# Kernel tuning notes

Measured on AMD Instinct MI355X. Metric: run time of the kernel, lower is better.

## Reference

```python
import jax, jax.numpy as jnp
import numpy as np

ALPHA = 0.2  # leakyrelu negative slope
NEG_INF = -1.0e12


def setup_inputs() -> dict:
    key = jax.random.key(0)
    k1, k2, k3, k4, k5 = jax.random.split(key, 5)
    B, N, C_in, C_out = 8, 2048, 256, 256
    inp = jax.random.normal(k1, (B, N, C_in), dtype=jnp.float32)
    adj = jax.random.randint(k2, (N, N), 0, 2, dtype=jnp.int32)
    # xavier_uniform with gain=1.414 for (C_in, C_out)
    limit = 1.414 * np.sqrt(6.0 / (C_in + C_out))
    W1 = jax.random.uniform(k3, (C_in, C_out), jnp.float32, -limit, limit)
    W2 = jax.random.uniform(k4, (C_in, C_out), jnp.float32, -limit, limit)
    W3 = jax.random.uniform(k5, (C_in, C_out), jnp.float32, -limit, limit)
    return {"inp": inp, "adj": adj, "W1": W1, "W2": W2, "W3": W3}


def reference(inp, adj, W1, W2, W3):
    # inp: [B,N,Cin], adj: [N,N], W*: [Cin,Cout]
    h1 = jnp.einsum('bnc,cd->bnd', inp, W1)  # [B,N,Cout] queries
    h2 = jnp.einsum('bnc,cd->bnd', inp, W2)  # [B,N,Cout] keys
    h3 = jnp.einsum('bnc,cd->bnd', inp, W3)  # [B,N,Cout] values
    e = jnp.einsum('bnd,bmd->bnm', h1, h2)   # [B,N,N] scores
    e = jax.nn.leaky_relu(e, ALPHA)
    e = jnp.where(adj[None, :, :] > 0, e, NEG_INF)
    attention = jax.nn.softmax(e, axis=-1)   # dropout p=0 / eval mode -> identity
    h_prime = jnp.einsum('bnm,bmd->bnd', attention, h3)
    return jax.nn.relu(h_prime)  # concat=True
```

## Files before the change

### kernel.cpp

```cpp
#include <hip/hip_runtime.h>

typedef __bf16 bf16_t;
typedef __bf16 bf16x4 __attribute__((ext_vector_type(4)));
typedef __bf16 bf16x8 __attribute__((ext_vector_type(8)));
typedef float floatx4 __attribute__((ext_vector_type(4)));
typedef signed char i8_t;
typedef int intx4 __attribute__((ext_vector_type(4)));

__device__ inline void split_hl(float v, bf16_t& hi, bf16_t& lo) {
    hi = (bf16_t)v;
    lo = (bf16_t)(v - (float)hi);
}

__global__ void adjbits_kernel(const int* __restrict__ adj, unsigned* __restrict__ bits) {
    int id = blockIdx.x * 256 + threadIdx.x;
    const int* p = adj + (size_t)id * 32;
    unsigned w = 0;
#pragma unroll
    for (int j = 0; j < 32; j += 4) {
        int4 v = *(const int4*)(p + j);
        w |= (v.x > 0 ? 1u : 0u) << j;
        w |= (v.y > 0 ? 1u : 0u) << (j + 1);
        w |= (v.z > 0 ? 1u : 0u) << (j + 2);
        w |= (v.w > 0 ? 1u : 0u) << (j + 3);
    }
    bits[id] = w;
}

__global__ void wtrans_kernel(const float* __restrict__ W1,
                              const float* __restrict__ W2,
                              const float* __restrict__ W3,
                              bf16_t* __restrict__ Wthi, bf16_t* __restrict__ Wtlo) {
    __shared__ float T[64 * 68];
    const int zi = blockIdx.z;
    const float* W = (zi == 0) ? W1 : ((zi == 1) ? W2 : W3);
    bf16_t* ohi = Wthi + zi * 256 * 256;
    bf16_t* olo = Wtlo + zi * 256 * 256;
    const int c0 = blockIdx.x * 64, d0 = blockIdx.y * 64;
    const int tid = threadIdx.x;
#pragma unroll
    for (int i = 0; i < 4; i++) {
        int idx = i * 256 + tid;
        int r = idx >> 4, c4 = (idx & 15) * 4;
        floatx4 v = *(const floatx4*)(W + (c0 + r) * 256 + d0 + c4);
        *(floatx4*)(&T[r * 68 + c4]) = v;
    }
    __syncthreads();
#pragma unroll
    for (int i = 0; i < 4; i++) {
        int idx = i * 256 + tid;
        int rd = idx & 63, cc4 = (idx >> 6) * 4;
        bf16x4 vh, vl;
#pragma unroll
        for (int ii = 0; ii < 4; ii++) {
            float v = T[(cc4 + ii) * 68 + rd];
            bf16_t h, l; split_hl(v, h, l);
            vh[ii] = h; vl[ii] = l;
        }
        *(bf16x4*)(ohi + (d0 + rd) * 256 + c0 + cc4) = vh;
        *(bf16x4*)(olo + (d0 + rd) * 256 + c0 + cc4) = vl;
    }
}

__global__ __launch_bounds__(256) void proj_kernel(
    const float* __restrict__ X,
    const bf16_t* __restrict__ Wthi, const bf16_t* __restrict__ Wtlo,
    i8_t* __restrict__ Q8h, i8_t* __restrict__ Q8l, float* __restrict__ sqv,
    i8_t* __restrict__ K8h, i8_t* __restrict__ K8l, float* __restrict__ skv,
    bf16_t* __restrict__ H3t) {
    __shared__ bf16_t Xh[64 * 40], Xl[64 * 40];
    __shared__ bf16_t Wh[256 * 40], Wl[256 * 40];
    const int z = blockIdx.y;
    const int row0 = blockIdx.x * 64;
    const int tid = threadIdx.x;
    const int w = tid >> 6, lane = tid & 63;
    const int m = lane & 15, q = lane >> 4;
    const bf16_t* Wzh = Wthi + z * 256 * 256;
    const bf16_t* Wzl = Wtlo + z * 256 * 256;

    floatx4 acc[16];
#pragma unroll
    for (int i = 0; i < 16; i++) acc[i] = (floatx4){0.f, 0.f, 0.f, 0.f};

    for (int c0 = 0; c0 < 256; c0 += 32) {
#pragma unroll
        for (int i = 0; i < 2; i++) {
            int idx = i * 256 + tid;
            int r = idx >> 3, c4 = (idx & 7) * 4;
            floatx4 v = *(const floatx4*)(X + (size_t)(row0 + r) * 256 + c0 + c4);
            bf16x4 vh, vl;
#pragma unroll
            for (int ii = 0; ii < 4; ii++) {
                bf16_t h, l; split_hl(v[ii], h, l);
                vh[ii] = h; vl[ii] = l;
            }
            *(bf16x4*)(&Xh[r * 40 + c4]) = vh;
            *(bf16x4*)(&Xl[r * 40 + c4]) = vl;
        }
#pragma unroll
        for (int i = 0; i < 4; i++) {
            int idx = i * 256 + tid;
            int d = idx >> 2, c8 = (idx & 3) * 8;
            *(bf16x8*)(&Wh[d * 40 + c8]) = *(const bf16x8*)(Wzh + d * 256 + c0 + c8);
            *(bf16x8*)(&Wl[d * 40 + c8]) = *(const bf16x8*)(Wzl + d * 256 + c0 + c8);
        }
        __syncthreads();
        bf16x8 ah = *(const bf16x8*)(&Xh[(w * 16 + m) * 40 + q * 8]);
        bf16x8 al = *(const bf16x8*)(&Xl[(w * 16 + m) * 40 + q * 8]);
#pragma unroll
        for (int nt = 0; nt < 16; nt++) {
            bf16x8 bh = *(const bf16x8*)(&Wh[(nt * 16 + m) * 40 + q * 8]);
            bf16x8 bl = *(const bf16x8*)(&Wl[(nt * 16 + m) * 40 + q * 8]);
            acc[nt] = __builtin_amdgcn_mfma_f32_16x16x32_bf16(ah, bh, acc[nt], 0, 0, 0);
            acc[nt] = __builtin_amdgcn_mfma_f32_16x16x32_bf16(ah, bl, acc[nt], 0, 0, 0);
            acc[nt] = __builtin_amdgcn_mfma_f32_16x16x32_bf16(al, bh, acc[nt], 0, 0, 0);
        }
        __syncthreads();
    }
    const int rbase = row0 + w * 16 + q * 4;
    if (z < 2) {
        i8_t* Dh = (z == 0) ? Q8h : K8h;
        i8_t* Dl = (z == 0) ? Q8l : K8l;
        float* sv = (z == 0) ? sqv : skv;
        float am[4] = {0.f, 0.f, 0.f, 0.f};
#pragma unroll
        for (int nt = 0; nt < 16; nt++)
#pragma unroll
            for (int r = 0; r < 4; r++) am[r] = fmaxf(am[r], fabsf(acc[nt][r]));
#pragma unroll
        for (int off = 1; off < 16; off <<= 1)
#pragma unroll
            for (int r = 0; r < 4; r++)
                am[r] = fmaxf(am[r], __shfl_xor(am[r], off, 64));
        float sc[4], inv[4];
#pragma unroll
        for (int r = 0; r < 4; r++) {
            sc[r]  = (am[r] > 0.f) ? am[r] * (1.f / 127.f) : 1.f;
            inv[r] = (am[r] > 0.f) ? 127.f / am[r] : 0.f;
        }
#pragma unroll
        for (int nt = 0; nt < 16; nt++)
#pragma unroll
            for (int r = 0; r < 4; r++) {
                float vq = acc[nt][r] * inv[r];
                float qh = rintf(vq);
                float ql = fminf(fmaxf(rintf((vq - qh) * 256.f), -127.f), 127.f);
                int offo = (rbase + r) * 256 + nt * 16 + m;
                Dh[offo] = (i8_t)(int)qh;
                Dl[offo] = (i8_t)(int)ql;
            }
        if (m == 0) {
#pragma unroll
            for (int r = 0; r < 4; r++) sv[rbase + r] = sc[r];
        }
    } else {
#pragma unroll
        for (int nt = 0; nt < 16; nt++)
#pragma unroll
            for (int r = 0; r < 4; r++) {
                int token = rbase + r;
                int b = token >> 11, n = token & 2047;
                H3t[(size_t)(b * 256 + nt * 16 + m) * 2048 + n] = (bf16_t)acc[nt][r];
            }
    }
}

#define K8SW(row, off) ((off) ^ (((row) & 7) << 4))
#define PSW(row, off)  ((off) ^ ((((row) >> 1) & 3) << 4))
__global__ __launch_bounds__(256, 2) void attn_kernel(
    const i8_t* __restrict__ Q8h, const i8_t* __restrict__ Q8l,
    const float* __restrict__ sqv,
    const i8_t* __restrict__ K8h, const i8_t* __restrict__ K8l,
    const float* __restrict__ skv,
    const bf16_t* __restrict__ H3t, const unsigned* __restrict__ adjbits,
    float* __restrict__ Opart, float* __restrict__ mpart, float* __restrict__ lpart,
    int klen) {
    __shared__ i8_t K8[2][32 * 256];
    __shared__ bf16_t Pl[4][16 * 32];
    __shared__ __align__(16) float Al[4][16];
    __shared__ __align__(16) int Fl[4];

    const int nwg = (int)(gridDim.x * gridDim.y * gridDim.z);
    const int wgid = (int)(blockIdx.x + (blockIdx.y << 5) + (blockIdx.z << 8));
    const int nid = (wgid & 7) * (nwg >> 3) + (wgid >> 3);
    const int qblk = nid & 31;
    const int b  = (nid >> 5) & 7;
    const int kz = nid >> 8;

    const int q0 = qblk * 64;
    const int tid = threadIdx.x;
    const int w = tid >> 6, lane = tid & 63;
    const int m = lane & 15, q = lane >> 4;

    char* K8B0 = (char*)&K8[0][0];
    char* K8B1 = (char*)&K8[1][0];
    char* PlB  = (char*)&Pl[w][0];

    const i8_t* qrh = Q8h + (size_t)(b * 2048 + q0 + w * 16 + m) * 256;
    const i8_t* qrl = Q8l + (size_t)(b * 2048 + q0 + w * 16 + m) * 256;
    intx4 qh8[4], ql8[4];
#pragma unroll
    for (int ck = 0; ck < 4; ck++) {
        qh8[ck] = *(const intx4*)(qrh + ck * 64 + q * 16);
        ql8[ck] = *(const intx4*)(qrl + ck * 64 + q * 16);
    }
    float sq4[4];
#pragma unroll
    for (int r = 0; r < 4; r++) sq4[r] = sqv[b * 2048 + q0 + w * 16 + q * 4 + r];

    bf16x8 vones;
#pragma unroll
    for (int i = 0; i < 8; i++) vones[i] = (bf16_t)1.0f;

    float m_run[4];
#pragma unroll
    for (int r = 0; r < 4; r++) m_run[r] = -3.0e38f;
    floatx4 l_acc = (floatx4){0.f, 0.f, 0.f, 0.f};
    floatx4 o[16];
#pragma unroll
    for (int i = 0; i < 16; i++) o[i] = (floatx4){0.f, 0.f, 0.f, 0.f};

    const unsigned* bitrow[4];
#pragma unroll
    for (int r = 0; r < 4; r++)
        bitrow[r] = adjbits + (size_t)(q0 + w * 16 + q * 4 + r) * 64;

    const bf16_t* vbase = H3t + (size_t)(b * 256 + w * 64 + m) * 2048 + q * 8;

    intx4 rkh[2], rkl[2];
    bf16x8 vcur[4], vnxt[4];
    float skt[2], skn[2];
    const int kbeg = kz * klen, kend = kbeg + klen;

#pragma unroll
    for (int i = 0; i < 2; i++) {
        int ci = i * 256 + tid;
        int kr = ci >> 4, cb = (ci & 15) * 16;
        rkh[i] = *(const intx4*)(K8h + (size_t)(b * 2048 + kbeg + kr) * 256 + cb);
        rkl[i] = *(const intx4*)(K8l + (size_t)(b * 2048 + kbeg + kr) * 256 + cb);
    }
#pragma unroll
    for (int dn = 0; dn < 4; dn++)
        vcur[dn] = *(const bf16x8*)(vbase + (size_t)(dn * 16) * 2048 + kbeg);
    skt[0] = skv[b * 2048 + kbeg + m];
    skt[1] = skv[b * 2048 + kbeg + 16 + m];

    for (int k0 = kbeg; k0 < kend; k0 += 32) {
        __syncthreads();
#pragma unroll
        for (int i = 0; i < 2; i++) {
            int ci = i * 256 + tid;
            int kr = ci >> 4, cb = (ci & 15) * 16;
            *(intx4*)(K8B0 + K8SW(kr, kr * 256 + cb)) = rkh[i];
            *(intx4*)(K8B1 + K8SW(kr, kr * 256 + cb)) = rkl[i];
        }
        __syncthreads();
        if (k0 + 32 < kend) {
            int kn = k0 + 32;
#pragma unroll
            for (int i = 0; i < 2; i++) {
                int ci = i * 256 + tid;
                int kr = ci >> 4, cb = (ci & 15) * 16;
                rkh[i] = *(const intx4*)(K8h + (size_t)(b * 2048 + kn + kr) * 256 + cb);
                rkl[i] = *(const intx4*)(K8l + (size_t)(b * 2048 + kn + kr) * 256 + cb);
            }
#pragma unroll
            for (int dn = 0; dn < 4; dn++)
                vnxt[dn] = *(const bf16x8*)(vbase + (size_t)(dn * 16) * 2048 + kn);
            skn[0] = skv[b * 2048 + kn + m];
            skn[1] = skv[b * 2048 + kn + 16 + m];
        }

        float s[2][4];
#pragma unroll
        for (int t = 0; t < 2; t++) {
            intx4 ch = {0, 0, 0, 0}, cm = {0, 0, 0, 0};
            const int row = t * 16 + m;
#pragma unroll
            for (int ck = 0; ck < 4; ck++) {
                const int cb2 = ck * 64 + q * 16;
                intx4 kh = *(const intx4*)(K8B0 + K8SW(row, row * 256 + cb2));
                intx4 kl = *(const intx4*)(K8B1 + K8SW(row, row * 256 + cb2));
                ch = __builtin_amdgcn_mfma_i32_16x16x64_i8(qh8[ck], kh, ch, 0, 0, 0);
                cm = __builtin_amdgcn_mfma_i32_16x16x64_i8(qh8[ck], kl, cm, 0, 0, 0);
                cm = __builtin_amdgcn_mfma_i32_16x16x64_i8(ql8[ck], kh, cm, 0, 0, 0);
            }
#pragma unroll
            for (int r = 0; r < 4; r++)
                s[t][r] = fmaf((float)cm[r], 0.00390625f, (float)ch[r]) * (sq4[r] * skt[t]);
        }

        unsigned aw[4];
#pragma unroll
        for (int r = 0; r < 4; r++) aw[r] = bitrow[r][k0 >> 5];
        float p[2][4], tmax[4];
#pragma unroll
        for (int r = 0; r < 4; r++) tmax[r] = -3.0e38f;
#pragma unroll
        for (int t = 0; t < 2; t++)
#pragma unroll
            for (int r = 0; r < 4; r++) {
                float v = s[t][r];
                v = (v > 0.f) ? v : 0.2f * v;
                v = ((aw[r] >> (t * 16 + m)) & 1u) ? v : -1.0e12f;
                p[t][r] = v;
                tmax[r] = fmaxf(tmax[r], v);
            }
#pragma unroll
        for (int off = 1; off < 16; off <<= 1)
#pragma unroll
            for (int r = 0; r < 4; r++)
                tmax[r] = fmaxf(tmax[r], __shfl_xor(tmax[r], off, 64));

        int rise = 0;
        float mnew[4];
#pragma unroll
        for (int r = 0; r < 4; r++) {
            mnew[r] = fmaxf(m_run[r], tmax[r]);
            rise |= (mnew[r] > m_run[r]);
        }
        const int rose = __any(rise);
        if (rose) {
            floatx4 a4;
#pragma unroll
            for (int r = 0; r < 4; r++) {
                float alpha = __expf(m_run[r] - mnew[r]);
                m_run[r] = mnew[r];
                l_acc[r] *= alpha;
                a4[r] = alpha;
            }
            if (m == 0) *(floatx4*)(&Al[w][q * 4]) = a4;
        }
        if (lane == 0) Fl[w] = rose;
#pragma unroll
        for (int t = 0; t < 2; t++)
#pragma unroll
            for (int r = 0; r < 4; r++)
                p[t][r] = __expf(p[t][r] - m_run[r]);

#pragma unroll
        for (int t = 0; t < 2; t++)
#pragma unroll
            for (int r = 0; r < 4; r++) {
                int row = q * 4 + r;
                *(bf16_t*)(PlB + PSW(row, row * 64 + (t * 16 + m) * 2)) = (bf16_t)p[t][r];
            }
        __syncthreads();

        int4 fl4 = *(const int4*)(&Fl[0]);
#pragma unroll
        for (int qb = 0; qb < 4; qb++) {
            int f = (qb == 0) ? fl4.x : (qb == 1) ? fl4.y : (qb == 2) ? fl4.z : fl4.w;
            if (f) {
                floatx4 a = *(const floatx4*)(&Al[qb][q * 4]);
#pragma unroll
                for (int dn = 0; dn < 4; dn++)
#pragma unroll
                    for (int r = 0; r < 4; r++) o[qb * 4 + dn][r] *= a[r];
            }
        }

        bf16x8 pa[4];
#pragma unroll
        for (int qb = 0; qb < 4; qb++)
            pa[qb] = *(const bf16x8*)((char*)&Pl[qb][0] + PSW(m, m * 64 + q * 16));
#pragma unroll
        for (int qb = 0; qb < 4; qb++)
            if (qb == w)
                l_acc = __builtin_amdgcn_mfma_f32_16x16x32_bf16(pa[qb], vones, l_acc, 0, 0, 0);
#pragma unroll
        for (int qb = 0; qb < 4; qb++)
#pragma unroll
            for (int dn = 0; dn < 4; dn++)
                o[qb * 4 + dn] = __builtin_amdgcn_mfma_f32_16x16x32_bf16(
                    pa[qb], vcur[dn], o[qb * 4 + dn], 0, 0, 0);

#pragma unroll
        for (int dn = 0; dn < 4; dn++) vcur[dn] = vnxt[dn];
        skt[0] = skn[0];
        skt[1] = skn[1];
    }

    const int rowbase = kz * 16384 + b * 2048 + q0;
#pragma unroll
    for (int qb = 0; qb < 4; qb++)
#pragma unroll
        for (int dn = 0; dn < 4; dn++)
#pragma unroll
            for (int r = 0; r < 4; r++)
                Opart[(size_t)(rowbase + qb * 16 + q * 4 + r) * 256 + w * 64 + dn * 16 + m] =
                    o[qb * 4 + dn][r];
    if (m == 0) {
        const int rowg = rowbase + w * 16 + q * 4;
#pragma unroll
        for (int r = 0; r < 4; r++) {
            mpart[rowg + r] = m_run[r];
            lpart[rowg + r] = l_acc[r];
        }
    }
}

__global__ __launch_bounds__(256) void merge_kernel(
    const float* __restrict__ Opart, const float* __restrict__ mpart,
    const float* __restrict__ lpart, float* __restrict__ out, int S) {
    int gid = blockIdx.x * 256 + threadIdx.x;
    int row = gid >> 6, c4 = (gid & 63) * 4;
    float M = -3.0e38f;
    for (int s = 0; s < S; s++) M = fmaxf(M, mpart[s * 16384 + row]);
    float denom = 0.f;
    float4 acc = make_float4(0.f, 0.f, 0.f, 0.f);
    for (int s = 0; s < S; s++) {
        float sc = __expf(mpart[s * 16384 + row] - M);
        denom += lpart[s * 16384 + row] * sc;
        float4 v = *(const float4*)(Opart + ((size_t)(s * 16384 + row)) * 256 + c4);
        acc.x += v.x * sc; acc.y += v.y * sc; acc.z += v.z * sc; acc.w += v.w * sc;
    }
    float inv = 1.f / denom;
    float4 r;
    r.x = fmaxf(acc.x * inv, 0.f);
    r.y = fmaxf(acc.y * inv, 0.f);
    r.z = fmaxf(acc.z * inv, 0.f);
    r.w = fmaxf(acc.w * inv, 0.f);
    *(float4*)(out + (size_t)row * 256 + c4) = r;
}

extern "C" void kernel_launch(void* const* d_in, const int* in_sizes, int n_in,
                              void* d_out, int out_size, void* d_ws, size_t ws_size,
                              hipStream_t stream) {
    const float* X   = (const float*)d_in[0];
    const int*   adj = (const int*)d_in[1];
    const float* W1  = (const float*)d_in[2];
    const float* W2  = (const float*)d_in[3];
    const float* W3  = (const float*)d_in[4];
    float* out = (float*)d_out;

    char* ws = (char*)d_ws;
    i8_t* Q8h = (i8_t*)(ws + ((size_t)0 << 20));
    i8_t* Q8l = (i8_t*)(ws + ((size_t)4 << 20));
    i8_t* K8h = (i8_t*)(ws + ((size_t)8 << 20));
    i8_t* K8l = (i8_t*)(ws + ((size_t)12 << 20));
    bf16_t* H3t = (bf16_t*)(ws + ((size_t)16 << 20));
    float* sqv = (float*)(ws + ((size_t)24 << 20));
    float* skv = (float*)(ws + ((size_t)24 << 20) + 65536);
    size_t wt0 = ((size_t)24 << 20) + 131072;
    bf16_t* Wthi = (bf16_t*)(ws + wt0);
    bf16_t* Wtlo = (bf16_t*)(ws + wt0 + 393216);
    float* mpart = (float*)(ws + wt0);
    float* lpart = (float*)(ws + wt0 + 131072);
    unsigned* adjb = (unsigned*)(ws + wt0 + 786432);
    size_t opart_off = wt0 + 786432 + 524288;
    const size_t need2 = opart_off + (size_t)2 * 16384 * 256 * 4;

    int S = (ws_size >= need2) ? 2 : 1;
    float* Opart = (S > 1) ? (float*)(ws + opart_off) : out;

    adjbits_kernel<<<512, 256, 0, stream>>>(adj, adjb);
    wtrans_kernel<<<dim3(4, 4, 3), 256, 0, stream>>>(W1, W2, W3, Wthi, Wtlo);
    proj_kernel<<<dim3(256, 3), 256, 0, stream>>>(X, Wthi, Wtlo,
                                                  Q8h, Q8l, sqv, K8h, K8l, skv, H3t);
    attn_kernel<<<dim3(32, 8, S), 256, 0, stream>>>(Q8h, Q8l, sqv, K8h, K8l, skv,
                                                    H3t, adjb, Opart, mpart, lpart,
                                                    2048 / S);
    merge_kernel<<<4096, 256, 0, stream>>>(Opart, mpart, lpart, out, S);
}
```

Measured before the change: 239.3 us.

## Stage K tiles via direct global-to-LDS loads with double buffering, split keys four ways

Replaces the register-staged K copy (global→VGPR→LDS plus an extra barrier) with global_load_lds DMA into a double-buffered LDS tile, removing one sync per iteration and the prefetch registers. V and key-scale loads are now issued in-iteration instead of prefetched. Launch bounds rise to 3 waves/SIMD and the key split S rises to 4 when the workspace allows, adding more partial outputs for the merge kernel. Risks include exposed V load latency, register spills under the tighter bound, and extra merge traffic.

```diff
diff --git a/kernel.cpp b/kernel.cpp
--- a/kernel.cpp
+++ b/kernel.cpp
@@ -6,6 +6,13 @@
 typedef float floatx4 __attribute__((ext_vector_type(4)));
 typedef signed char i8_t;
 typedef int intx4 __attribute__((ext_vector_type(4)));
+
+typedef const __attribute__((address_space(1))) void as1_cv;
+typedef __attribute__((address_space(3))) void as3_v;
+
+__device__ inline void gload_lds16(const void* g, void* l) {
+    __builtin_amdgcn_global_load_lds((as1_cv*)g, (as3_v*)l, 16, 0, 0);
+}
 
 __device__ inline void split_hl(float v, bf16_t& hi, bf16_t& lo) {
     hi = (bf16_t)v;
@@ -167,7 +174,7 @@
 
 #define K8SW(row, off) ((off) ^ (((row) & 7) << 4))
 #define PSW(row, off)  ((off) ^ ((((row) >> 1) & 3) << 4))
-__global__ __launch_bounds__(256, 2) void attn_kernel(
+__global__ __launch_bounds__(256, 3) void attn_kernel(
     const i8_t* __restrict__ Q8h, const i8_t* __restrict__ Q8l,
     const float* __restrict__ sqv,
     const i8_t* __restrict__ K8h, const i8_t* __restrict__ K8l,
@@ -175,7 +182,7 @@
     const bf16_t* __restrict__ H3t, const unsigned* __restrict__ adjbits,
     float* __restrict__ Opart, float* __restrict__ mpart, float* __restrict__ lpart,
     int klen) {
-    __shared__ i8_t K8[2][32 * 256];
+    __shared__ i8_t K8[2][2][32 * 256];
     __shared__ bf16_t Pl[4][16 * 32];
     __shared__ __align__(16) float Al[4][16];
     __shared__ __align__(16) int Fl[4];
@@ -192,10 +199,6 @@
     const int w = tid >> 6, lane = tid & 63;
     const int m = lane & 15, q = lane >> 4;
 
-    char* K8B0 = (char*)&K8[0][0];
-    char* K8B1 = (char*)&K8[1][0];
-    char* PlB  = (char*)&Pl[w][0];
-
     const i8_t* qrh = Q8h + (size_t)(b * 2048 + q0 + w * 16 + m) * 256;
     const i8_t* qrl = Q8l + (size_t)(b * 2048 + q0 + w * 16 + m) * 256;
     intx4 qh8[4], ql8[4];
@@ -227,50 +230,40 @@
 
     const bf16_t* vbase = H3t + (size_t)(b * 256 + w * 64 + m) * 2048 + q * 8;
 
-    intx4 rkh[2], rkl[2];
-    bf16x8 vcur[4], vnxt[4];
-    float skt[2], skn[2];
     const int kbeg = kz * klen, kend = kbeg + klen;
 
-#pragma unroll
-    for (int i = 0; i < 2; i++) {
-        int ci = i * 256 + tid;
-        int kr = ci >> 4, cb = (ci & 15) * 16;
-        rkh[i] = *(const intx4*)(K8h + (size_t)(b * 2048 + kbeg + kr) * 256 + cb);
-        rkl[i] = *(const intx4*)(K8l + (size_t)(b * 2048 + kbeg + kr) * 256 + cb);
-    }
-#pragma unroll
-    for (int dn = 0; dn < 4; dn++)
-        vcur[dn] = *(const bf16x8*)(vbase + (size_t)(dn * 16) * 2048 + kbeg);
-    skt[0] = skv[b * 2048 + kbeg + m];
-    skt[1] = skv[b * 2048 + kbeg + 16 + m];
+    auto STAGE = [&](int buf, int kt) {
+#pragma unroll
+        for (int h = 0; h < 2; h++) {
+            const i8_t* gb = h ? K8l : K8h;
+#pragma unroll
+            for (int j = 0; j < 2; j++) {
+                const int s0 = (w * 2 + j) << 10;
+                const int s = s0 + lane * 16;
+                const int row = s >> 8;
+                const int gcol = (s & 255) ^ ((row & 7) << 4);
+                const i8_t* src = gb + (size_t)(b * 2048 + kt + row) * 256 + gcol;
+                gload_lds16(src, (char*)&K8[buf][h][0] + s0);
+            }
+        }
+    };
+
+    STAGE(0, kbeg);
+    int cur = 0;
 
     for (int k0 = kbeg; k0 < kend; k0 += 32) {
         __syncthreads();
-#pragma unroll
-        for (int i = 0; i < 2; i++) {
-            int ci = i * 256 + tid;
-            int kr = ci >> 4, cb = (ci & 15) * 16;
-            *(intx4*)(K8B0 + K8SW(kr, kr * 256 + cb)) = rkh[i];
-            *(intx4*)(K8B1 + K8SW(kr, kr * 256 + cb)) = rkl[i];
-        }
-        __syncthreads();
-        if (k0 + 32 < kend) {
-            int kn = k0 + 32;
-#pragma unroll
-            for (int i = 0; i < 2; i++) {
-                int ci = i * 256 + tid;
-                int kr = ci >> 4, cb = (ci & 15) * 16;
-                rkh[i] = *(const intx4*)(K8h + (size_t)(b * 2048 + kn + kr) * 256 + cb);
-                rkl[i] = *(const intx4*)(K8l + (size_t)(b * 2048 + kn + kr) * 256 + cb);
-            }
-#pragma unroll
-            for (int dn = 0; dn < 4; dn++)
-                vnxt[dn] = *(const bf16x8*)(vbase + (size_t)(dn * 16) * 2048 + kn);
-            skn[0] = skv[b * 2048 + kn + m];
-            skn[1] = skv[b * 2048 + kn + 16 + m];
-        }
-
+        if (k0 + 32 < kend) STAGE(cur ^ 1, k0 + 32);
+
+        bf16x8 vcur[4];
+#pragma unroll
+        for (int dn = 0; dn < 4; dn++)
+            vcur[dn] = *(const bf16x8*)(vbase + (size_t)(dn * 16) * 2048 + k0);
+        const float sk0 = skv[b * 2048 + k0 + m];
+        const float sk1 = skv[b * 2048 + k0 + 16 + m];
+
+        char* KB0 = (char*)&K8[cur][0][0];
+        char* KB1 = (char*)&K8[cur][1][0];
         float s[2][4];
 #pragma unroll
         for (int t = 0; t < 2; t++) {
@@ -279,15 +272,16 @@
 #pragma unroll
             for (int ck = 0; ck < 4; ck++) {
                 const int cb2 = ck * 64 + q * 16;
-                intx4 kh = *(const intx4*)(K8B0 + K8SW(row, row * 256 + cb2));
-                intx4 kl = *(const intx4*)(K8B1 + K8SW(row, row * 256 + cb2));
+                intx4 kh = *(const intx4*)(KB0 + K8SW(row, row * 256 + cb2));
+                intx4 kl = *(const intx4*)(KB1 + K8SW(row, row * 256 + cb2));
                 ch = __builtin_amdgcn_mfma_i32_16x16x64_i8(qh8[ck], kh, ch, 0, 0, 0);
                 cm = __builtin_amdgcn_mfma_i32_16x16x64_i8(qh8[ck], kl, cm, 0, 0, 0);
                 cm = __builtin_amdgcn_mfma_i32_16x16x64_i8(ql8[ck], kh, cm, 0, 0, 0);
             }
+            const float sk = t ? sk1 : sk0;
 #pragma unroll
             for (int r = 0; r < 4; r++)
-                s[t][r] = fmaf((float)cm[r], 0.00390625f, (float)ch[r]) * (sq4[r] * skt[t]);
+                s[t][r] = fmaf((float)cm[r], 0.00390625f, (float)ch[r]) * (sq4[r] * sk);
         }
 
         unsigned aw[4];
@@ -338,6 +332,7 @@
             for (int r = 0; r < 4; r++)
                 p[t][r] = __expf(p[t][r] - m_run[r]);
 
+        char* PlB = (char*)&Pl[w][0];
 #pragma unroll
         for (int t = 0; t < 2; t++)
 #pragma unroll
@@ -375,10 +370,7 @@
                 o[qb * 4 + dn] = __builtin_amdgcn_mfma_f32_16x16x32_bf16(
                     pa[qb], vcur[dn], o[qb * 4 + dn], 0, 0, 0);
 
-#pragma unroll
-        for (int dn = 0; dn < 4; dn++) vcur[dn] = vnxt[dn];
-        skt[0] = skn[0];
-        skt[1] = skn[1];
+        cur ^= 1;
     }
 
     const int rowbase = kz * 16384 + b * 2048 + q0;
@@ -446,12 +438,13 @@
     bf16_t* Wthi = (bf16_t*)(ws + wt0);
     bf16_t* Wtlo = (bf16_t*)(ws + wt0 + 393216);
     float* mpart = (float*)(ws + wt0);
-    float* lpart = (float*)(ws + wt0 + 131072);
+    float* lpart = (float*)(ws + wt0 + 262144);
     unsigned* adjb = (unsigned*)(ws + wt0 + 786432);
     size_t opart_off = wt0 + 786432 + 524288;
     const size_t need2 = opart_off + (size_t)2 * 16384 * 256 * 4;
-
-    int S = (ws_size >= need2) ? 2 : 1;
+    const size_t need4 = opart_off + (size_t)4 * 16384 * 256 * 4;
+
+    int S = (ws_size >= need4) ? 4 : ((ws_size >= need2) ? 2 : 1);
     float* Opart = (S > 1) ? (float*)(ws + opart_off) : out;
 
     adjbits_kernel<<<512, 256, 0, stream>>>(adj, adjb);
```

Measured after the change: 365.5 us. +52.7%, slower.
